# Optimization experiments

Hardware: AMD Instinct MI355X
Metric: run time of the kernel (lower is better)

Reference implementation:

```python
import jax, jax.numpy as jnp
import numpy as np

IN_FEAT = 3 * 299 * 299  # 268203
D1 = 512
H = 28
OUT = 2


def setup_inputs() -> dict:
    key = jax.random.key(0)
    ks = jax.random.split(key, 10)
    B, T = 4, 64
    s1 = 1.0 / np.sqrt(IN_FEAT)
    s2 = 1.0 / np.sqrt(D1)
    s3 = 1.0 / np.sqrt(H)
    return {
        "x": jax.random.normal(ks[0], (B, T, 3, 299, 299), jnp.float32),
        "W1": jax.random.uniform(ks[1], (IN_FEAT, D1), jnp.float32, -s1, s1),
        "b1": jax.random.uniform(ks[2], (D1,), jnp.float32, -s1, s1),
        "Wi": jax.random.uniform(ks[3], (D1, H), jnp.float32, -s2, s2),
        "Wr": jax.random.uniform(ks[4], (H, H), jnp.float32, -s3, s3),
        "br": jax.random.uniform(ks[5], (H,), jnp.float32, -s3, s3),
        "A": jax.random.normal(ks[6], (H,), jnp.float32),
        "tau": 1.0 + jax.random.uniform(ks[7], (H,), jnp.float32),  # positive time constants
        "W2": jax.random.uniform(ks[8], (H, OUT), jnp.float32, -s3, s3),
        "b2": jax.random.uniform(ks[9], (OUT,), jnp.float32, -s3, s3),
    }


def reference(x, W1, b1, Wi, Wr, br, A, tau, W2, b2):
    B, T = x.shape[0], x.shape[1]
    xf = x.reshape(B, T, -1)                      # [B, T, 268203]
    h1 = jax.nn.relu(jnp.einsum('btf,fd->btd', xf, W1) + b1)  # [B, T, 512]
    u = jnp.einsum('btd,dh->bth', h1, Wi)         # precomputed input drive [B, T, H]
    dt = 1.0

    def step(h, u_t):
        # fused-Euler LTC cell: f gates both time-constant and attractor A
        ft = jax.nn.sigmoid(u_t + h @ Wr + br)
        h_new = (h + dt * ft * A) / (1.0 + dt * (1.0 / tau + ft))
        return h_new, h_new

    h0 = jnp.zeros((B, H), x.dtype)
    _, hs = jax.lax.scan(step, h0, jnp.swapaxes(u, 0, 1))  # [T, B, H]
    last = jax.nn.relu(hs[-1])                    # relu then take last step
    out = last @ W2 + b2                          # [B, 2]
    return jax.nn.sigmoid(out)
```

## Files before the change

### kernel.cpp

```cpp
#include <hip/hip_runtime.h>
#include <hip/hip_bf16.h>

#define KTOT   268203
#define MROWS  256
#define NCOLS  512
#define HDIM   28
#define NSTEPS 8382
#define FSTEP  8381

typedef __attribute__((ext_vector_type(4))) float  f32x4;
typedef __attribute__((ext_vector_type(8))) __bf16 bf16x8;

#define AUX_NT 2

static __device__ inline bf16x8 pack8(const float* f) {
    union { bf16x8 v; __hip_bfloat16 h[8]; } u;
    #pragma unroll
    for (int j = 0; j < 8; ++j) u.h[j] = __float2bfloat16(f[j]);
    return u.v;
}

__global__ __launch_bounds__(512, 2) void gemm1_kernel(
    const float* __restrict__ x, const float* __restrict__ W1,
    float* __restrict__ part, int steps_per, int nks)
{
    __shared__ __align__(16) float Albuf[3][MROWS * 32];
    __shared__ __align__(16) float Bbuf[3][32 * 128];

    const int tid  = threadIdx.x;
    const int lane = tid & 63;
    const int w    = tid >> 6;
    const int wm   = w >> 1;
    const int wn   = w & 1;

    int bx, ks;
    {
        const int id = blockIdx.x;
        if ((nks & 7) == 0) {
            const int xcd  = id & 7;
            const int rest = id >> 3;
            bx = rest & 3;
            ks = ((rest >> 2) << 3) | xcd;
        } else {
            bx = id & 3;
            ks = id >> 2;
        }
    }
    const int bcol = bx * 128;

    const int dlt = lane >> 5;
    const int m   = lane & 31;
    const int rw7 = (2 * w + dlt) & 7;
    const int ag  = (m >> 2) ^ rw7;
    const size_t a_off = (size_t)(2 * w + dlt) * KTOT + ag * 4 + (m & 3);
    const size_t b_off = (size_t)(2 * w + dlt) * NCOLS + bcol + m * 4;

    f32x4 acc[4][4];
    #pragma unroll
    for (int i = 0; i < 4; ++i)
        #pragma unroll
        for (int j = 0; j < 4; ++j)
            acc[i][j] = (f32x4){0.f, 0.f, 0.f, 0.f};

    const int s0 = ks * steps_per;
    int s1 = s0 + steps_per;
    if (s1 > NSTEPS) s1 = NSTEPS;

    auto issue_step = [&](int s, int buf) {
        const float* ap = x + a_off + (size_t)s * 32;
        #pragma unroll
        for (int i = 0; i < 16; ++i) {
            const float* gp = ap + (size_t)i * 16 * KTOT;
            char* lp = (char*)&Albuf[buf][0] + (i * 8 + w) * 256;
            __builtin_amdgcn_global_load_lds(
                (const __attribute__((address_space(1))) unsigned int*)(const void*)gp,
                (__attribute__((address_space(3))) unsigned int*)(void*)lp, 4, 0, 0);
        }
        const float* bp = W1 + b_off + (size_t)s * 32 * NCOLS;
        #pragma unroll
        for (int i = 0; i < 2; ++i) {
            const float* gp = bp + (size_t)i * 16 * NCOLS;
            char* lp = (char*)&Bbuf[buf][0] + (i * 512 + w * 64) * 16;
            __builtin_amdgcn_global_load_lds(
                (const __attribute__((address_space(1))) unsigned int*)(const void*)gp,
                (__attribute__((address_space(3))) unsigned int*)(void*)lp, 16, 0, AUX_NT);
        }
    };

    auto compute = [&](int buf) {
        const int rc = lane & 15, ko = lane >> 4;
        bf16x8 bq[4];
        #pragma unroll
        for (int ni = 0; ni < 4; ++ni) {
            const int colL = wn * 64 + ni * 16 + rc;
            float bf[8];
            #pragma unroll
            for (int j = 0; j < 8; ++j)
                bf[j] = Bbuf[buf][(ko * 8 + j) * 128 + colL];
            bq[ni] = pack8(bf);
        }
        const int soff = ((2 * ko) ^ (rc & 7)) * 16;
        #pragma unroll
        for (int mi = 0; mi < 4; ++mi) {
            const int ab = (wm * 64 + mi * 16 + rc) * 128;
            float afv[8];
            *(f32x4*)&afv[0] = *(const f32x4*)((const char*)&Albuf[buf][0] + ab + soff);
            *(f32x4*)&afv[4] = *(const f32x4*)((const char*)&Albuf[buf][0] + ab + (soff ^ 16));
            const bf16x8 af = pack8(afv);
            #pragma unroll
            for (int ni = 0; ni < 4; ++ni)
                acc[mi][ni] = __builtin_amdgcn_mfma_f32_16x16x32_bf16(
                    af, bq[ni], acc[mi][ni], 0, 0, 0);
        }
    };

    const int s1f  = (s1 < FSTEP) ? s1 : FSTEP;
    const int nfull = s1f - s0;
    if (nfull > 0) {
        issue_step(s0, 0);
        if (nfull > 1) issue_step(s0 + 1, 1);
        for (int t = 0; t < nfull; ++t) {
            if (t + 1 < nfull) { asm volatile("s_waitcnt vmcnt(18)" ::: "memory"); }
            else               { asm volatile("s_waitcnt vmcnt(0)"  ::: "memory"); }
            __builtin_amdgcn_s_barrier();
            __builtin_amdgcn_sched_barrier(0);
            compute(t % 3);
            if (t + 2 < nfull) issue_step(s0 + t + 2, (t + 2) % 3);
        }
    }

    if (s1 > FSTEP) {
        const int buf = nfull % 3;
        {
            const int arow0 = tid >> 5, ak = tid & 31;
            const int gg = ak >> 2, jj = ak & 3;
            #pragma unroll
            for (int i = 0; i < 16; ++i) {
                const int row = arow0 + i * 16;
                const float v = (ak < (KTOT - FSTEP * 32))
                    ? x[(size_t)row * KTOT + (size_t)FSTEP * 32 + ak] : 0.f;
                Albuf[buf][row * 32 + (gg ^ (row & 7)) * 4 + jj] = v;
            }
        }
        {
            const int bc2 = tid & 127, bkg2 = tid >> 7;
            #pragma unroll
            for (int j = 0; j < 8; ++j) {
                const int k = bkg2 * 8 + j;
                const float v = (k < (KTOT - FSTEP * 32))
                    ? W1[(size_t)(FSTEP * 32 + k) * NCOLS + bcol + bc2] : 0.f;
                Bbuf[buf][k * 128 + bc2] = v;
            }
        }
        __syncthreads();
        compute(buf);
    }

    float* outp = part + (size_t)ks * MROWS * NCOLS;
    #pragma unroll
    for (int mi = 0; mi < 4; ++mi) {
        const int r0 = wm * 64 + mi * 16 + ((lane >> 4) * 4);
        #pragma unroll
        for (int ni = 0; ni < 4; ++ni) {
            const int c = bcol + wn * 64 + ni * 16 + (lane & 15);
            #pragma unroll
            for (int j = 0; j < 4; ++j)
                outp[(size_t)(r0 + j) * NCOLS + c] = acc[mi][ni][j];
        }
    }
}

__global__ __launch_bounds__(512) void reduce_u_kernel(
    const float* __restrict__ part, const float* __restrict__ b1,
    const float* __restrict__ Wi, float* __restrict__ u, int nks)
{
    __shared__ float h1[NCOLS];
    __shared__ f32x4 red[4][128];
    const int row = blockIdx.x;
    const int tid = threadIdx.x;
    const int c4  = tid & 127;
    const int kk  = tid >> 7;

    f32x4 sum = (f32x4){0.f, 0.f, 0.f, 0.f};
    for (int k = kk; k < nks; k += 4)
        sum += *(const f32x4*)&part[((size_t)k * MROWS + row) * NCOLS + c4 * 4];
    red[kk][c4] = sum;
    __syncthreads();

    if (tid < 128) {
        f32x4 t = red[0][tid] + red[1][tid] + red[2][tid] + red[3][tid];
        const f32x4 bb = *(const f32x4*)&b1[tid * 4];
        t += bb;
        #pragma unroll
        for (int j = 0; j < 4; ++j) h1[tid * 4 + j] = fmaxf(t[j], 0.f);
    }
    __syncthreads();

    const int wv = tid >> 6, lane = tid & 63;
    #pragma unroll
    for (int hh = 0; hh < 4; ++hh) {
        const int h = wv * 4 + hh;
        if (h < HDIM) {
            float p = 0.f;
            #pragma unroll
            for (int dd = 0; dd < 8; ++dd) {
                const int d = lane + dd * 64;
                p += h1[d] * Wi[d * HDIM + h];
            }
            #pragma unroll
            for (int off = 32; off; off >>= 1) p += __shfl_down(p, off);
            if (lane == 0) u[row * HDIM + h] = p;
        }
    }
}

__global__ __launch_bounds__(64) void recur_kernel(
    const float* __restrict__ u, const float* __restrict__ Wr,
    const float* __restrict__ br, const float* __restrict__ Av,
    const float* __restrict__ tau, const float* __restrict__ W2,
    const float* __restrict__ b2, float* __restrict__ out)
{
    const int b = blockIdx.x;
    const int j = threadIdx.x;
    const bool act = j < HDIM;
    const int jj = act ? j : 0;

    float wr[HDIM];
    #pragma unroll
    for (int i = 0; i < HDIM; ++i) wr[i] = act ? Wr[i * HDIM + jj] : 0.f;
    const float brj = act ? br[jj] : 0.f;
    const float Aj  = act ? Av[jj] : 0.f;
    const float itj = act ? (1.f / tau[jj]) : 0.f;

    float uv[64];
    #pragma unroll
    for (int t = 0; t < 64; ++t)
        uv[t] = act ? u[(b * 64 + t) * HDIM + jj] : 0.f;

    float h = 0.f;
    #pragma unroll
    for (int t = 0; t < 64; ++t) {
        float a = uv[t] + brj;
        #pragma unroll
        for (int i = 0; i < HDIM; ++i)
            a += __shfl(h, i) * wr[i];
        const float ft = 1.f / (1.f + expf(-a));
        const float hn = (h + ft * Aj) / (1.f + itj + ft);
        h = act ? hn : 0.f;
    }

    const float r  = act ? fmaxf(h, 0.f) : 0.f;
    float p0 = act ? r * W2[jj * 2 + 0] : 0.f;
    float p1 = act ? r * W2[jj * 2 + 1] : 0.f;
    #pragma unroll
    for (int off = 32; off; off >>= 1) {
        p0 += __shfl_down(p0, off);
        p1 += __shfl_down(p1, off);
    }
    if (j == 0) {
        out[b * 2 + 0] = 1.f / (1.f + expf(-(p0 + b2[0])));
        out[b * 2 + 1] = 1.f / (1.f + expf(-(p1 + b2[1])));
    }
}

extern "C" void kernel_launch(void* const* d_in, const int* in_sizes, int n_in,
                              void* d_out, int out_size, void* d_ws, size_t ws_size,
                              hipStream_t stream)
{
    (void)in_sizes; (void)n_in; (void)out_size;
    const float* x   = (const float*)d_in[0];
    const float* W1  = (const float*)d_in[1];
    const float* b1  = (const float*)d_in[2];
    const float* Wi  = (const float*)d_in[3];
    const float* Wr  = (const float*)d_in[4];
    const float* br  = (const float*)d_in[5];
    const float* Av  = (const float*)d_in[6];
    const float* tau = (const float*)d_in[7];
    const float* W2  = (const float*)d_in[8];
    const float* b2  = (const float*)d_in[9];
    float* out = (float*)d_out;

    const size_t per_split = (size_t)MROWS * NCOLS * sizeof(float);
    int nks = 64;
    while (nks > 8 && (size_t)nks * per_split + (1 << 16) > ws_size) nks -= 8;
    const int steps_per = (NSTEPS + nks - 1) / nks;

    float* part = (float*)d_ws;
    float* u    = part + (size_t)nks * MROWS * NCOLS;

    gemm1_kernel<<<dim3(4 * nks), 512, 0, stream>>>(x, W1, part, steps_per, nks);
    reduce_u_kernel<<<dim3(MROWS), 512, 0, stream>>>(part, b1, Wi, u, nks);
    recur_kernel<<<dim3(4), 64, 0, stream>>>(u, Wr, br, Av, tau, W2, b2, out);
}
```

Measured before the change: 269.7 us.

## Widen GEMM tile to 256 columns, double-buffer, store bf16 split-K partials

Each block of the split-K GEMM now covers 256 output columns instead of 128, so every x tile loaded feeds twice as many MFMAs and the number of column blocks drops from 4 to 2. Pipelining goes from triple to double buffering with a full vmcnt(0) wait each step. Split-K partials are written and reduced in bf16, which halves partial traffic and allows 128 K-splits. In exchange the partial sums lose precision, the wider accumulator raises register pressure, and the shallower prefetch may expose load latency.

```diff
diff --git a/kernel.cpp b/kernel.cpp
--- a/kernel.cpp
+++ b/kernel.cpp
@@ -7,6 +7,8 @@
 #define HDIM   28
 #define NSTEPS 8382
 #define FSTEP  8381
+#define KREM   11
+#define BN     256
 
 typedef __attribute__((ext_vector_type(4))) float  f32x4;
 typedef __attribute__((ext_vector_type(8))) __bf16 bf16x8;
@@ -19,13 +21,17 @@
     for (int j = 0; j < 8; ++j) u.h[j] = __float2bfloat16(f[j]);
     return u.v;
 }
+static __device__ inline unsigned short bfbits(float v) {
+    __hip_bfloat16 h = __float2bfloat16(v);
+    union { __hip_bfloat16 h; unsigned short u; } c; c.h = h; return c.u;
+}
 
 __global__ __launch_bounds__(512, 2) void gemm1_kernel(
     const float* __restrict__ x, const float* __restrict__ W1,
-    float* __restrict__ part, int steps_per, int nks)
+    __hip_bfloat16* __restrict__ part, int steps_per, int nks)
 {
-    __shared__ __align__(16) float Albuf[3][MROWS * 32];
-    __shared__ __align__(16) float Bbuf[3][32 * 128];
+    __shared__ __align__(16) float Albuf[2][MROWS * 32];
+    __shared__ __align__(16) float Bbuf[2][32 * BN];
 
     const int tid  = threadIdx.x;
     const int lane = tid & 63;
@@ -37,34 +43,37 @@
     {
         const int id = blockIdx.x;
         if ((nks & 7) == 0) {
-            const int xcd  = id & 7;
-            const int rest = id >> 3;
-            bx = rest & 3;
-            ks = ((rest >> 2) << 3) | xcd;
+            const int xcd = id & 7;
+            const int m_  = id >> 3;
+            bx = m_ & 1;
+            ks = ((m_ >> 1) << 3) | xcd;
         } else {
-            bx = id & 3;
-            ks = id >> 2;
-        }
-    }
-    const int bcol = bx * 128;
+            bx = id & 1;
+            ks = id >> 1;
+        }
+    }
+    const int bcol = bx * BN;
 
     const int dlt = lane >> 5;
     const int m   = lane & 31;
     const int rw7 = (2 * w + dlt) & 7;
     const int ag  = (m >> 2) ^ rw7;
     const size_t a_off = (size_t)(2 * w + dlt) * KTOT + ag * 4 + (m & 3);
-    const size_t b_off = (size_t)(2 * w + dlt) * NCOLS + bcol + m * 4;
-
-    f32x4 acc[4][4];
+    const size_t b_off = bcol + (size_t)(lane) * 4;
+
+    f32x4 acc[4][8];
     #pragma unroll
     for (int i = 0; i < 4; ++i)
         #pragma unroll
-        for (int j = 0; j < 4; ++j)
+        for (int j = 0; j < 8; ++j)
             acc[i][j] = (f32x4){0.f, 0.f, 0.f, 0.f};
 
     const int s0 = ks * steps_per;
     int s1 = s0 + steps_per;
     if (s1 > NSTEPS) s1 = NSTEPS;
+    int s1f = (s1 < FSTEP) ? s1 : FSTEP;
+    int nfull = s1f - s0;
+    if (nfull < 0) nfull = 0;
 
     auto issue_step = [&](int s, int buf) {
         const float* ap = x + a_off + (size_t)s * 32;
@@ -78,9 +87,9 @@
         }
         const float* bp = W1 + b_off + (size_t)s * 32 * NCOLS;
         #pragma unroll
-        for (int i = 0; i < 2; ++i) {
-            const float* gp = bp + (size_t)i * 16 * NCOLS;
-            char* lp = (char*)&Bbuf[buf][0] + (i * 512 + w * 64) * 16;
+        for (int i = 0; i < 4; ++i) {
+            const float* gp = bp + (size_t)(i * 8 + w) * NCOLS;
+            char* lp = (char*)&Bbuf[buf][0] + (i * 8 + w) * 1024;
             __builtin_amdgcn_global_load_lds(
                 (const __attribute__((address_space(1))) unsigned int*)(const void*)gp,
                 (__attribute__((address_space(3))) unsigned int*)(void*)lp, 16, 0, AUX_NT);
@@ -89,14 +98,14 @@
 
     auto compute = [&](int buf) {
         const int rc = lane & 15, ko = lane >> 4;
-        bf16x8 bq[4];
-        #pragma unroll
-        for (int ni = 0; ni < 4; ++ni) {
-            const int colL = wn * 64 + ni * 16 + rc;
+        bf16x8 bq[8];
+        #pragma unroll
+        for (int ni = 0; ni < 8; ++ni) {
+            const int colL = wn * 128 + ni * 16 + rc;
             float bf[8];
             #pragma unroll
             for (int j = 0; j < 8; ++j)
-                bf[j] = Bbuf[buf][(ko * 8 + j) * 128 + colL];
+                bf[j] = Bbuf[buf][(ko * 8 + j) * BN + colL];
             bq[ni] = pack8(bf);
         }
         const int soff = ((2 * ko) ^ (rc & 7)) * 16;
@@ -108,70 +117,74 @@
             *(f32x4*)&afv[4] = *(const f32x4*)((const char*)&Albuf[buf][0] + ab + (soff ^ 16));
             const bf16x8 af = pack8(afv);
             #pragma unroll
-            for (int ni = 0; ni < 4; ++ni)
+            for (int ni = 0; ni < 8; ++ni)
                 acc[mi][ni] = __builtin_amdgcn_mfma_f32_16x16x32_bf16(
                     af, bq[ni], acc[mi][ni], 0, 0, 0);
         }
     };
 
-    const int s1f  = (s1 < FSTEP) ? s1 : FSTEP;
-    const int nfull = s1f - s0;
     if (nfull > 0) {
         issue_step(s0, 0);
-        if (nfull > 1) issue_step(s0 + 1, 1);
         for (int t = 0; t < nfull; ++t) {
-            if (t + 1 < nfull) { asm volatile("s_waitcnt vmcnt(18)" ::: "memory"); }
-            else               { asm volatile("s_waitcnt vmcnt(0)"  ::: "memory"); }
+            asm volatile("s_waitcnt vmcnt(0)" ::: "memory");
             __builtin_amdgcn_s_barrier();
             __builtin_amdgcn_sched_barrier(0);
-            compute(t % 3);
-            if (t + 2 < nfull) issue_step(s0 + t + 2, (t + 2) % 3);
-        }
-    }
-
-    if (s1 > FSTEP) {
-        const int buf = nfull % 3;
+            if (t + 1 < nfull) issue_step(s0 + t + 1, (t + 1) & 1);
+            compute(t & 1);
+        }
+    }
+
+    if (s1 > FSTEP && s0 < s1) {
+        const int buf = nfull & 1;
+        __syncthreads();
         {
-            const int arow0 = tid >> 5, ak = tid & 31;
-            const int gg = ak >> 2, jj = ak & 3;
+            const int row = tid >> 1, half = tid & 1;
             #pragma unroll
             for (int i = 0; i < 16; ++i) {
-                const int row = arow0 + i * 16;
-                const float v = (ak < (KTOT - FSTEP * 32))
-                    ? x[(size_t)row * KTOT + (size_t)FSTEP * 32 + ak] : 0.f;
-                Albuf[buf][row * 32 + (gg ^ (row & 7)) * 4 + jj] = v;
+                const int k = half * 16 + i;
+                const float v = (k < KREM)
+                    ? x[(size_t)row * KTOT + (size_t)FSTEP * 32 + k] : 0.f;
+                Albuf[buf][row * 32 + ((k >> 2) ^ (row & 7)) * 4 + (k & 3)] = v;
             }
         }
         {
-            const int bc2 = tid & 127, bkg2 = tid >> 7;
-            #pragma unroll
-            for (int j = 0; j < 8; ++j) {
-                const int k = bkg2 * 8 + j;
-                const float v = (k < (KTOT - FSTEP * 32))
-                    ? W1[(size_t)(FSTEP * 32 + k) * NCOLS + bcol + bc2] : 0.f;
-                Bbuf[buf][k * 128 + bc2] = v;
+            const int c = tid & 255, og = tid >> 8;
+            #pragma unroll
+            for (int i = 0; i < 16; ++i) {
+                const int k = og * 16 + i;
+                const float v = (k < KREM)
+                    ? W1[(size_t)(FSTEP * 32 + k) * NCOLS + bcol + c] : 0.f;
+                Bbuf[buf][k * BN + c] = v;
             }
         }
         __syncthreads();
         compute(buf);
     }
 
-    float* outp = part + (size_t)ks * MROWS * NCOLS;
+    __hip_bfloat16* outp = part + (size_t)ks * MROWS * NCOLS;
+    const int rc = lane & 15, q = lane >> 4;
     #pragma unroll
     for (int mi = 0; mi < 4; ++mi) {
-        const int r0 = wm * 64 + mi * 16 + ((lane >> 4) * 4);
-        #pragma unroll
-        for (int ni = 0; ni < 4; ++ni) {
-            const int c = bcol + wn * 64 + ni * 16 + (lane & 15);
-            #pragma unroll
-            for (int j = 0; j < 4; ++j)
-                outp[(size_t)(r0 + j) * NCOLS + c] = acc[mi][ni][j];
+        #pragma unroll
+        for (int ni = 0; ni < 8; ++ni) {
+            const int col = bcol + wn * 128 + ni * 16 + rc;
+            #pragma unroll
+            for (int j = 0; j < 4; ++j) {
+                const int row = wm * 64 + mi * 16 + q * 4 + j;
+                const float v  = acc[mi][ni][j];
+                const float vh = __shfl_xor(v, 1);
+                if (!(rc & 1)) {
+                    const unsigned int pk =
+                        (unsigned int)bfbits(v) | ((unsigned int)bfbits(vh) << 16);
+                    *(unsigned int*)(outp + (size_t)row * NCOLS + col) = pk;
+                }
+            }
         }
     }
 }
 
 __global__ __launch_bounds__(512) void reduce_u_kernel(
-    const float* __restrict__ part, const float* __restrict__ b1,
+    const __hip_bfloat16* __restrict__ part, const float* __restrict__ b1,
     const float* __restrict__ Wi, float* __restrict__ u, int nks)
 {
     __shared__ float h1[NCOLS];
@@ -181,9 +194,16 @@
     const int c4  = tid & 127;
     const int kk  = tid >> 7;
 
+    const unsigned short* pu = (const unsigned short*)part;
     f32x4 sum = (f32x4){0.f, 0.f, 0.f, 0.f};
-    for (int k = kk; k < nks; k += 4)
-        sum += *(const f32x4*)&part[((size_t)k * MROWS + row) * NCOLS + c4 * 4];
+    for (int k = kk; k < nks; k += 4) {
+        const size_t base = ((size_t)k * MROWS + row) * NCOLS + c4 * 4;
+        ushort4 pv = *(const ushort4*)&pu[base];
+        union { unsigned int u; float f; } c0, c1, c2, c3;
+        c0.u = (unsigned int)pv.x << 16; c1.u = (unsigned int)pv.y << 16;
+        c2.u = (unsigned int)pv.z << 16; c3.u = (unsigned int)pv.w << 16;
+        sum[0] += c0.f; sum[1] += c1.f; sum[2] += c2.f; sum[3] += c3.f;
+    }
     red[kk][c4] = sum;
     __syncthreads();
 
@@ -280,15 +300,15 @@
     const float* b2  = (const float*)d_in[9];
     float* out = (float*)d_out;
 
-    const size_t per_split = (size_t)MROWS * NCOLS * sizeof(float);
-    int nks = 64;
-    while (nks > 8 && (size_t)nks * per_split + (1 << 16) > ws_size) nks -= 8;
+    const size_t per_split = (size_t)MROWS * NCOLS * sizeof(__hip_bfloat16);
+    int nks = 128;
+    while (nks > 8 && (size_t)nks * per_split + (1 << 16) > ws_size) nks >>= 1;
     const int steps_per = (NSTEPS + nks - 1) / nks;
 
-    float* part = (float*)d_ws;
-    float* u    = part + (size_t)nks * MROWS * NCOLS;
-
-    gemm1_kernel<<<dim3(4 * nks), 512, 0, stream>>>(x, W1, part, steps_per, nks);
+    __hip_bfloat16* part = (__hip_bfloat16*)d_ws;
+    float* u = (float*)((char*)d_ws + (size_t)nks * per_split);
+
+    gemm1_kernel<<<dim3(2 * nks), 512, 0, stream>>>(x, W1, part, steps_per, nks);
     reduce_u_kernel<<<dim3(MROWS), 512, 0, stream>>>(part, b1, Wi, u, nks);
     recur_kernel<<<dim3(4), 64, 0, stream>>>(u, Wr, br, Av, tau, W2, b2, out);
 }
```

After: 282.3 us. 1.05x slower.
